# Performance work log

Measured on AMD Instinct MI355X. Metric: run time of the kernel, lower is better.

Reference implementation:

```python
import jax, jax.numpy as jnp
import numpy as np

N = 21  # nodes per graph (20 laser sectors + 1 robot node)
MAX_RANGE = 10.0
_bound = np.linspace(-np.pi / 2 - 0.03, np.pi / 2, 21, dtype=np.float32)[:-1]
_angles = _bound + np.float32(np.pi / 20)
ANGLE_FEAT = jnp.asarray(np.stack([np.sin(_angles), np.cos(_angles)], 1), dtype=jnp.float32)  # [20,2]


def _build_nodes(state24):
    # state24: [B,24] -> node features [B,21,7]
    B = state24.shape[0]
    laser = state24[:, :20, None] / MAX_RANGE                       # [B,20,1]
    angle = jnp.broadcast_to(ANGLE_FEAT[None], (B, 20, 2))          # [B,20,2]
    sector = jnp.concatenate([laser, angle, jnp.zeros((B, 20, 4), state24.dtype)], -1)  # [B,20,7]
    robot = jnp.concatenate([jnp.zeros((B, 1, 3), state24.dtype), state24[:, None, 20:]], -1)  # [B,1,7]
    return jnp.concatenate([sector, robot], axis=1)                 # [B,21,7]


def _gatv2(x, Wl, Wr, att, bias, heads, dim):
    # GATv2 over a fully-connected graph with self-loops (dense all-pairs).
    # e_ij = att . leaky_relu(Wl x_j + Wr x_i); alpha = softmax_j; out_i = sum_j alpha_ij (Wl x_j)
    B = x.shape[0]
    gl = (x @ Wl).reshape(B, N, heads, dim)  # source transform [B,j,H,D]
    gr = (x @ Wr).reshape(B, N, heads, dim)  # target transform [B,i,H,D]
    s = jax.nn.leaky_relu(gl[:, None] + gr[:, :, None], negative_slope=0.2)  # [B,i,j,H,D]
    e = jnp.einsum('bijhd,hd->bijh', s, att)                                  # [B,i,j,H]
    alpha = jax.nn.softmax(e, axis=2)                                          # softmax over sources j
    out = jnp.einsum('bijh,bjhd->bihd', alpha, gl).reshape(B, N, heads * dim)
    return out + bias


def setup_inputs() -> dict:
    key = jax.random.key(0)
    ks = jax.random.split(key, 16)
    r = lambda k, shape, s: (jax.random.normal(k, shape, dtype=jnp.float32) * s)
    B = 1024
    return {
        'state24': jax.random.normal(ks[0], (B, 24), dtype=jnp.float32),
        'Wl1': r(ks[1], (7, 256), 0.3), 'Wr1': r(ks[2], (7, 256), 0.3),
        'att1': r(ks[3], (4, 64), 0.1), 'b1': r(ks[4], (256,), 0.02),
        'Wl2': r(ks[5], (256, 64), 0.06), 'Wr2': r(ks[6], (256, 64), 0.06),
        'att2': r(ks[7], (1, 64), 0.1), 'b2': r(ks[8], (64,), 0.02),
        'fc1_w': r(ks[9], (64, 256), 0.12), 'fc1_b': r(ks[10], (256,), 0.02),
        'fc2_w': r(ks[11], (256, 256), 0.06), 'fc2_b': r(ks[12], (256,), 0.02),
        'fc3_w': r(ks[13], (256, 2), 0.06), 'fc3_b': r(ks[14], (2,), 0.02),
    }


def reference(state24, Wl1, Wr1, att1, b1, Wl2, Wr2, att2, b2,
              fc1_w, fc1_b, fc2_w, fc2_b, fc3_w, fc3_b):
    x = _build_nodes(state24)                               # [B,21,7]
    h = jax.nn.elu(_gatv2(x, Wl1, Wr1, att1, b1, 4, 64))    # [B,21,256]
    h = _gatv2(h, Wl2, Wr2, att2, b2, 1, 64)                # [B,21,64]
    nfv = jnp.mean(h, axis=1)                               # global_mean_pool -> [B,64]
    h = jax.nn.relu(nfv @ fc1_w + fc1_b)
    h = jax.nn.relu(h @ fc2_w + fc2_b)
    return jnp.tanh(h @ fc3_w + fc3_b)                      # [B,2]
```

## Files before the change

kernel.cpp:

```cpp
#include <hip/hip_runtime.h>
#include <hip/hip_fp16.h>
#include <math.h>

#define PI_D 3.141592653589793

typedef _Float16 h2 __attribute__((ext_vector_type(2)));
typedef _Float16 h8 __attribute__((ext_vector_type(8)));
typedef unsigned short us8 __attribute__((ext_vector_type(8)));
typedef __fp16 f16v2 __attribute__((ext_vector_type(2)));
typedef __fp16 f16v8 __attribute__((ext_vector_type(8)));
typedef float f32x4 __attribute__((ext_vector_type(4)));

#define STR1 264
#define STR2 66
#define STR2H 72
#define EPS 24
#define EPS2 24

static __device__ __forceinline__ h2 pack_h2(float a, float b) {
    return __builtin_bit_cast(h2, __builtin_amdgcn_cvt_pkrtz(a, b));
}

static __device__ __forceinline__ float fdot2(h2 a, h2 b, float c) {
    return __builtin_amdgcn_fdot2(__builtin_bit_cast(f16v2, a),
                                  __builtin_bit_cast(f16v2, b), c, false);
}

static __device__ __forceinline__ h8 habs8(h8 x) {
    us8 u = __builtin_bit_cast(us8, x);
    us8 m = {0x7fff, 0x7fff, 0x7fff, 0x7fff, 0x7fff, 0x7fff, 0x7fff, 0x7fff};
    return __builtin_bit_cast(h8, (us8)(u & m));
}

static __device__ __forceinline__ f32x4 mfma16(h8 a, h8 b, f32x4 c) {
    return __builtin_amdgcn_mfma_f32_16x16x32_f16(
        __builtin_bit_cast(f16v8, a), __builtin_bit_cast(f16v8, b), c, 0, 0, 0);
}

__global__ __launch_bounds__(256) void pack_weights_kernel(
    const float* __restrict__ Wl2, const float* __restrict__ Wr2,
    const float* __restrict__ fc1_w, const float* __restrict__ fc2_w,
    h8* __restrict__ ws)
{
    int idx = blockIdx.x * 256 + threadIdx.x;
    if (idx < 4096) {
        const float* W = idx < 2048 ? Wl2 : Wr2;
        int t = idx & 2047;
        int ntile = t >> 9, rem = t & 511;
        int kchunk = rem >> 6, lane = rem & 63;
        int n = ntile * 16 + (lane & 15);
        int k0 = kchunk * 32 + (lane >> 4) * 8;
        h8 o;
        #pragma unroll
        for (int j = 0; j < 8; ++j) o[j] = (_Float16)W[(k0 + j) * 64 + n];
        ws[idx] = o;
    } else if (idx < 6144) {
        int t = idx - 4096;
        int k2 = t >> 6, c = t & 63;
        h8 o;
        #pragma unroll
        for (int q = 0; q < 4; ++q) {
            o[2 * q]     = (_Float16)fc1_w[(2 * k2) * 256 + 4 * c + q];
            o[2 * q + 1] = (_Float16)fc1_w[(2 * k2 + 1) * 256 + 4 * c + q];
        }
        ws[idx] = o;
    } else {
        int t = idx - 6144;
        int k2 = t >> 6, c = t & 63;
        h8 o;
        #pragma unroll
        for (int q = 0; q < 4; ++q) {
            o[2 * q]     = (_Float16)fc2_w[(2 * k2) * 256 + 4 * c + q];
            o[2 * q + 1] = (_Float16)fc2_w[(2 * k2 + 1) * 256 + 4 * c + q];
        }
        ws[idx] = o;
    }
}

__global__ __launch_bounds__(256, 4) void actor_fused_kernel(
    const float* __restrict__ state24,
    const float* __restrict__ Wl1, const float* __restrict__ Wr1,
    const float* __restrict__ att1, const float* __restrict__ b1,
    const float* __restrict__ att2, const float* __restrict__ b2,
    const float* __restrict__ fc1_b, const float* __restrict__ fc2_b,
    const float* __restrict__ fc3_w, const float* __restrict__ fc3_b,
    const h8* __restrict__ wsL, const h8* __restrict__ wsR,
    const h8* __restrict__ wsF1, const h8* __restrict__ wsF2,
    float* __restrict__ out, int B)
{
    const int bix = blockIdx.x;
    if (bix >= B) return;
    const int tid = threadIdx.x;

    __shared__ float sinL[20], cosL[20], laserL[20], robotL[4];
    __shared__ __align__(16) h2 attLh[128];
    __shared__ __align__(16) h2 att2Lh[32];
    __shared__ __align__(16) _Float16 gr1h[22 * STR1];
    __shared__ __align__(16) union {
        struct { _Float16 gl1h[21 * STR1];
                 float eP[84 * EPS];
                 float uv[168]; } p1;
        struct { float gl2[24 * STR2];
                 _Float16 gl2h[24 * STR2H];
                 _Float16 gr2h[24 * STR2H];
                 float e2[24 * EPS2];
                 float u2v2[42];
                 float red[4][256];
                 _Float16 nfvh[64]; _Float16 hah[256]; _Float16 hbh[256]; } p2;
    } U;

    if (tid < 20) {
        double step = (PI_D + 0.03) / 20.0;
        float bound = (float)(-PI_D / 2.0 - 0.03 + (double)tid * step);
        float ang = bound + (float)(PI_D / 20.0);
        sinL[tid] = sinf(ang);
        cosL[tid] = cosf(ang);
        laserL[tid] = state24[bix * 24 + tid] * 0.1f;
    }
    if (tid >= 32 && tid < 36) robotL[tid - 32] = state24[bix * 24 + 20 + (tid - 32)];
    if (tid < 128) {
        float2 ap = ((const float2*)att1)[tid];
        attLh[tid] = pack_h2(0.4f * ap.x, 0.4f * ap.y);
    }
    if (tid >= 128 && tid < 160) {
        float2 ap = ((const float2*)att2)[tid - 128];
        att2Lh[tid - 128] = pack_h2(0.4f * ap.x, 0.4f * ap.y);
    }
    __syncthreads();

    {
        const int d2 = tid & 127;
        const int half = tid >> 7;
        float2 wl[7], wr[7];
        #pragma unroll
        for (int k = 0; k < 7; k++) {
            wl[k] = ((const float2*)Wl1)[k * 128 + d2];
            wr[k] = ((const float2*)Wr1)[k * 128 + d2];
        }
        const int base = half * 11;
        #pragma unroll
        for (int nn = 0; nn < 11; ++nn) {
            int node = base + nn;
            if (node < 21) {
                float a0, a1, b0, b1v;
                if (node < 20) {
                    float l = laserL[node], s = sinL[node], c = cosL[node];
                    a0 = l * wl[0].x + s * wl[1].x + c * wl[2].x;
                    a1 = l * wl[0].y + s * wl[1].y + c * wl[2].y;
                    b0 = l * wr[0].x + s * wr[1].x + c * wr[2].x;
                    b1v = l * wr[0].y + s * wr[1].y + c * wr[2].y;
                } else {
                    float r0 = robotL[0], r1 = robotL[1], r2 = robotL[2], r3 = robotL[3];
                    a0 = r0 * wl[3].x + r1 * wl[4].x + r2 * wl[5].x + r3 * wl[6].x;
                    a1 = r0 * wl[3].y + r1 * wl[4].y + r2 * wl[5].y + r3 * wl[6].y;
                    b0 = r0 * wr[3].x + r1 * wr[4].x + r2 * wr[5].x + r3 * wr[6].x;
                    b1v = r0 * wr[3].y + r1 * wr[4].y + r2 * wr[5].y + r3 * wr[6].y;
                }
                ((h2*)(U.p1.gl1h + node * STR1))[d2] = pack_h2(a0, a1);
                ((h2*)(gr1h + node * STR1))[d2] = pack_h2(b0, b1v);
            }
        }
    }
    __syncthreads();

    if (tid < 168) {
        int r = tid < 84 ? tid : tid - 84;
        int h = r / 21, idx = r - h * 21;
        const _Float16* rowp = (tid < 84 ? U.p1.gl1h : gr1h) + idx * STR1 + h * 64;
        const h8* row8 = (const h8*)rowp;
        const h2* ar = attLh + h * 32;
        float l0 = 0.f, l1 = 0.f;
        #pragma unroll
        for (int ch = 0; ch < 8; ++ch) {
            h8 g = row8[ch];
            l0 = fdot2(__builtin_shufflevector(g, g, 0, 1), ar[ch * 4 + 0], l0);
            l1 = fdot2(__builtin_shufflevector(g, g, 2, 3), ar[ch * 4 + 1], l1);
            l0 = fdot2(__builtin_shufflevector(g, g, 4, 5), ar[ch * 4 + 2], l0);
            l1 = fdot2(__builtin_shufflevector(g, g, 6, 7), ar[ch * 4 + 3], l1);
        }
        U.p1.uv[tid] = l0 + l1;
    }
    __syncthreads();

    {
        const int h = tid >> 6;
        const int lane = tid & 63;
        h2 ar[32];
        #pragma unroll
        for (int q = 0; q < 32; ++q) ar[q] = attLh[h * 32 + q];

        for (int it = 0; it < 7; ++it) {
            int q = it * 64 + lane;
            if (q < 441) {
                int i = q / 21;
                int j = q - i * 21;
                const h8* gA8 = (const h8*)(U.p1.gl1h + j * STR1 + h * 64);
                const h8* gB8 = (const h8*)(gr1h + i * STR1 + h * 64);
                float m0 = 0.f, m1 = 0.f;
                #pragma unroll
                for (int ch = 0; ch < 8; ++ch) {
                    h8 x = gA8[ch] + gB8[ch];
                    h8 ax = habs8(x);
                    m0 = fdot2(__builtin_shufflevector(ax, ax, 0, 1), ar[ch * 4 + 0], m0);
                    m1 = fdot2(__builtin_shufflevector(ax, ax, 2, 3), ar[ch * 4 + 1], m1);
                    m0 = fdot2(__builtin_shufflevector(ax, ax, 4, 5), ar[ch * 4 + 2], m0);
                    m1 = fdot2(__builtin_shufflevector(ax, ax, 6, 7), ar[ch * 4 + 3], m1);
                }
                U.p1.eP[(h * 21 + i) * EPS + j] = m0 + m1;
            }
        }
    }
    __syncthreads();

    if (tid < 84) {
        int h = tid / 21, i = tid - h * 21;
        float* row = U.p1.eP + tid * EPS;
        const float* uu = U.p1.uv + h * 21;
        float vi = 1.5f * U.p1.uv[84 + h * 21 + i];
        float ebuf[21];
        float m = -1e30f;
        #pragma unroll
        for (int j = 0; j < 21; j++) {
            float e = row[j] + 1.5f * uu[j] + vi;
            ebuf[j] = e;
            m = fmaxf(m, e);
        }
        float s = 0.f;
        #pragma unroll
        for (int j = 0; j < 21; j++) { float v = __expf(ebuf[j] - m); ebuf[j] = v; s += v; }
        float r = 1.f / s;
        #pragma unroll
        for (int j = 0; j < 21; j++) row[j] = ebuf[j] * r;
    }
    __syncthreads();

    {
        if (tid < 33) {
            h8 zz = {(_Float16)0.f, (_Float16)0.f, (_Float16)0.f, (_Float16)0.f,
                     (_Float16)0.f, (_Float16)0.f, (_Float16)0.f, (_Float16)0.f};
            ((h8*)gr1h)[21 * 33 + tid] = zz;
        }
        const int h = tid >> 6, c = tid & 63;
        const int col = h * 64 + c;
        float glv[21];
        #pragma unroll
        for (int j = 0; j < 21; ++j) glv[j] = (float)U.p1.gl1h[j * STR1 + col];
        float bb = b1[col];
        for (int i = 0; i < 21; ++i) {
            const float4* ar4 = (const float4*)(U.p1.eP + (h * 21 + i) * EPS);
            float4 q0 = ar4[0], q1 = ar4[1], q2 = ar4[2], q3 = ar4[3], q4 = ar4[4];
            float a20 = U.p1.eP[(h * 21 + i) * EPS + 20];
            float acc;
            acc = q0.x * glv[0];
            acc = fmaf(q0.y, glv[1], acc);
            acc = fmaf(q0.z, glv[2], acc);
            acc = fmaf(q0.w, glv[3], acc);
            acc = fmaf(q1.x, glv[4], acc);
            acc = fmaf(q1.y, glv[5], acc);
            acc = fmaf(q1.z, glv[6], acc);
            acc = fmaf(q1.w, glv[7], acc);
            acc = fmaf(q2.x, glv[8], acc);
            acc = fmaf(q2.y, glv[9], acc);
            acc = fmaf(q2.z, glv[10], acc);
            acc = fmaf(q2.w, glv[11], acc);
            acc = fmaf(q3.x, glv[12], acc);
            acc = fmaf(q3.y, glv[13], acc);
            acc = fmaf(q3.z, glv[14], acc);
            acc = fmaf(q3.w, glv[15], acc);
            acc = fmaf(q4.x, glv[16], acc);
            acc = fmaf(q4.y, glv[17], acc);
            acc = fmaf(q4.z, glv[18], acc);
            acc = fmaf(q4.w, glv[19], acc);
            acc = fmaf(a20, glv[20], acc);
            float v = acc + bb;
            v = v > 0.f ? v : __expf(v) - 1.f;
            gr1h[i * STR1 + col] = (_Float16)v;
        }
    }
    __syncthreads();

    {
        const int lane = tid & 63;
        const int w = tid >> 6;
        const int mrow = lane & 15;
        const int quad = lane >> 4;
        int rowA1 = 16 + mrow; if (rowA1 > 21) rowA1 = 21;
        const h8* hA0 = (const h8*)(gr1h + mrow * STR1 + quad * 8);
        const h8* hA1 = (const h8*)(gr1h + rowA1 * STR1 + quad * 8);
        const h8* bL = wsL + w * 512 + lane;
        const h8* bR = wsR + w * 512 + lane;
        f32x4 aL0 = {0.f, 0.f, 0.f, 0.f}, aL1 = {0.f, 0.f, 0.f, 0.f};
        f32x4 aR0 = {0.f, 0.f, 0.f, 0.f}, aR1 = {0.f, 0.f, 0.f, 0.f};
        #pragma unroll
        for (int kc = 0; kc < 8; ++kc) {
            h8 A0 = hA0[kc * 4];
            h8 A1 = hA1[kc * 4];
            h8 BL = bL[kc * 64];
            h8 BR = bR[kc * 64];
            aL0 = mfma16(A0, BL, aL0);
            aL1 = mfma16(A1, BL, aL1);
            aR0 = mfma16(A0, BR, aR0);
            aR1 = mfma16(A1, BR, aR1);
        }
        const int col = w * 16 + mrow;
        #pragma unroll
        for (int r = 0; r < 4; ++r) {
            int row0 = quad * 4 + r;
            U.p2.gl2[row0 * STR2 + col] = aL0[r];
            U.p2.gl2h[row0 * STR2H + col] = (_Float16)aL0[r];
            U.p2.gr2h[row0 * STR2H + col] = (_Float16)aR0[r];
            int row1 = 16 + row0;
            if (row1 < 21) {
                U.p2.gl2[row1 * STR2 + col] = aL1[r];
                U.p2.gl2h[row1 * STR2H + col] = (_Float16)aL1[r];
                U.p2.gr2h[row1 * STR2H + col] = (_Float16)aR1[r];
            }
        }
    }
    __syncthreads();

    {
        h2 ar2[32];
        #pragma unroll
        for (int q = 0; q < 32; ++q) ar2[q] = att2Lh[q];

        #pragma unroll
        for (int it = 0; it < 2; ++it) {
            int t = it * 256 + tid;
            if (t < 441) {
                int i = t / 21;
                int j = t - i * 21;
                const h8* gA8 = (const h8*)(U.p2.gl2h + j * STR2H);
                const h8* gB8 = (const h8*)(U.p2.gr2h + i * STR2H);
                float m0 = 0.f, m1 = 0.f;
                #pragma unroll
                for (int ch = 0; ch < 8; ++ch) {
                    h8 x = gA8[ch] + gB8[ch];
                    h8 ax = habs8(x);
                    m0 = fdot2(__builtin_shufflevector(ax, ax, 0, 1), ar2[ch * 4 + 0], m0);
                    m1 = fdot2(__builtin_shufflevector(ax, ax, 2, 3), ar2[ch * 4 + 1], m1);
                    m0 = fdot2(__builtin_shufflevector(ax, ax, 4, 5), ar2[ch * 4 + 2], m0);
                    m1 = fdot2(__builtin_shufflevector(ax, ax, 6, 7), ar2[ch * 4 + 3], m1);
                }
                U.p2.e2[i * EPS2 + j] = m0 + m1;
            } else if (t < 483) {
                int u = t - 441;
                int r = u < 21 ? u : u - 21;
                const _Float16* rowp = (u < 21 ? U.p2.gl2h : U.p2.gr2h) + r * STR2H;
                const h8* row8 = (const h8*)rowp;
                float l0 = 0.f, l1 = 0.f;
                #pragma unroll
                for (int ch = 0; ch < 8; ++ch) {
                    h8 g = row8[ch];
                    l0 = fdot2(__builtin_shufflevector(g, g, 0, 1), ar2[ch * 4 + 0], l0);
                    l1 = fdot2(__builtin_shufflevector(g, g, 2, 3), ar2[ch * 4 + 1], l1);
                    l0 = fdot2(__builtin_shufflevector(g, g, 4, 5), ar2[ch * 4 + 2], l0);
                    l1 = fdot2(__builtin_shufflevector(g, g, 6, 7), ar2[ch * 4 + 3], l1);
                }
                U.p2.u2v2[u] = l0 + l1;
            }
        }
    }
    __syncthreads();

    if (tid < 24) {
        float* row = U.p2.e2 + tid * EPS2;
        if (tid < 21) {
            const float* uu = U.p2.u2v2;
            float vi = 1.5f * U.p2.u2v2[21 + tid];
            float ebuf[21];
            float m = -1e30f;
            #pragma unroll
            for (int j = 0; j < 21; j++) {
                float e = row[j] + 1.5f * uu[j] + vi;
                ebuf[j] = e;
                m = fmaxf(m, e);
            }
            float s = 0.f;
            #pragma unroll
            for (int j = 0; j < 21; j++) { float v = __expf(ebuf[j] - m); ebuf[j] = v; s += v; }
            float r = 1.f / s;
            #pragma unroll
            for (int j = 0; j < 21; j++) row[j] = ebuf[j] * r;
        } else {
            #pragma unroll
            for (int j = 0; j < 21; j++) row[j] = 0.f;
        }
    }
    __syncthreads();

    {
        int d = tid & 63, g = tid >> 6;
        float glv2[21];
        #pragma unroll
        for (int j = 0; j < 21; ++j) glv2[j] = U.p2.gl2[j * STR2 + d];
        float sacc = 0.f;
        #pragma unroll
        for (int m = 0; m < 6; ++m) {
            int i = g + 4 * m;
            const float4* ar4 = (const float4*)(U.p2.e2 + i * EPS2);
            float4 q0 = ar4[0], q1 = ar4[1], q2 = ar4[2], q3 = ar4[3], q4 = ar4[4];
            float a20 = U.p2.e2[i * EPS2 + 20];
            float acc;
            acc = q0.x * glv2[0];
            acc = fmaf(q0.y, glv2[1], acc);
            acc = fmaf(q0.z, glv2[2], acc);
            acc = fmaf(q0.w, glv2[3], acc);
            acc = fmaf(q1.x, glv2[4], acc);
            acc = fmaf(q1.y, glv2[5], acc);
            acc = fmaf(q1.z, glv2[6], acc);
            acc = fmaf(q1.w, glv2[7], acc);
            acc = fmaf(q2.x, glv2[8], acc);
            acc = fmaf(q2.y, glv2[9], acc);
            acc = fmaf(q2.z, glv2[10], acc);
            acc = fmaf(q2.w, glv2[11], acc);
            acc = fmaf(q3.x, glv2[12], acc);
            acc = fmaf(q3.y, glv2[13], acc);
            acc = fmaf(q3.z, glv2[14], acc);
            acc = fmaf(q3.w, glv2[15], acc);
            acc = fmaf(q4.x, glv2[16], acc);
            acc = fmaf(q4.y, glv2[17], acc);
            acc = fmaf(q4.z, glv2[18], acc);
            acc = fmaf(q4.w, glv2[19], acc);
            acc = fmaf(a20, glv2[20], acc);
            sacc += acc;
        }
        U.p2.red[g][d] = sacc;
    }
    __syncthreads();
    if (tid < 64) {
        float v = (U.p2.red[0][tid] + U.p2.red[1][tid] + U.p2.red[2][tid] + U.p2.red[3][tid])
                  * (1.f / 21.f) + b2[tid];
        U.p2.nfvh[tid] = (_Float16)v;
    }
    __syncthreads();

    {
        int c = tid & 63, g = tid >> 6;
        const h2* x2p = (const h2*)U.p2.nfvh;
        float4 acc = {0.f, 0.f, 0.f, 0.f};
        #pragma unroll
        for (int kk = 0; kk < 8; ++kk) {
            int k2 = g * 8 + kk;
            h8 w = wsF1[k2 * 64 + c];
            h2 x2 = x2p[k2];
            acc.x = fdot2(__builtin_shufflevector(w, w, 0, 1), x2, acc.x);
            acc.y = fdot2(__builtin_shufflevector(w, w, 2, 3), x2, acc.y);
            acc.z = fdot2(__builtin_shufflevector(w, w, 4, 5), x2, acc.z);
            acc.w = fdot2(__builtin_shufflevector(w, w, 6, 7), x2, acc.w);
        }
        ((float4*)U.p2.red[g])[c] = acc;
    }
    __syncthreads();
    {
        float v = U.p2.red[0][tid] + U.p2.red[1][tid] + U.p2.red[2][tid] + U.p2.red[3][tid]
                  + fc1_b[tid];
        U.p2.hah[tid] = (_Float16)fmaxf(v, 0.f);
    }
    __syncthreads();

    {
        int c = tid & 63, g = tid >> 6;
        const h8* haH = (const h8*)U.p2.hah;
        float4 acc = {0.f, 0.f, 0.f, 0.f};
#define FC2_STEP(q, p)                                                          \
        {                                                                       \
            int k2 = g * 32 + (q) * 4 + (p);                                    \
            h8 w = wsF2[k2 * 64 + c];                                           \
            h2 x2 = __builtin_shufflevector(xa, xa, 2 * (p), 2 * (p) + 1);      \
            acc.x = fdot2(__builtin_shufflevector(w, w, 0, 1), x2, acc.x);      \
            acc.y = fdot2(__builtin_shufflevector(w, w, 2, 3), x2, acc.y);      \
            acc.z = fdot2(__builtin_shufflevector(w, w, 4, 5), x2, acc.z);      \
            acc.w = fdot2(__builtin_shufflevector(w, w, 6, 7), x2, acc.w);      \
        }
        #pragma unroll
        for (int q = 0; q < 8; ++q) {
            h8 xa = haH[g * 8 + q];
            FC2_STEP(q, 0)
            FC2_STEP(q, 1)
            FC2_STEP(q, 2)
            FC2_STEP(q, 3)
        }
#undef FC2_STEP
        ((float4*)U.p2.red[g])[c] = acc;
    }
    __syncthreads();
    {
        float v = U.p2.red[0][tid] + U.p2.red[1][tid] + U.p2.red[2][tid] + U.p2.red[3][tid]
                  + fc2_b[tid];
        U.p2.hbh[tid] = (_Float16)fmaxf(v, 0.f);
    }
    __syncthreads();

    if (tid < 128) {
        int o = tid >> 6, l = tid & 63;
        float s = 0.f;
        #pragma unroll
        for (int m = 0; m < 4; m++) {
            int k = l + 64 * m;
            s = fmaf((float)U.p2.hbh[k], fc3_w[k * 2 + o], s);
        }
        #pragma unroll
        for (int off = 32; off >= 1; off >>= 1) s += __shfl_down(s, off, 64);
        if (l == 0) out[bix * 2 + o] = tanhf(s + fc3_b[o]);
    }
}

extern "C" void kernel_launch(void* const* d_in, const int* in_sizes, int n_in,
                              void* d_out, int out_size, void* d_ws, size_t ws_size,
                              hipStream_t stream) {
    const float* state24 = (const float*)d_in[0];
    const float* Wl1 = (const float*)d_in[1];
    const float* Wr1 = (const float*)d_in[2];
    const float* att1 = (const float*)d_in[3];
    const float* b1 = (const float*)d_in[4];
    const float* Wl2 = (const float*)d_in[5];
    const float* Wr2 = (const float*)d_in[6];
    const float* att2 = (const float*)d_in[7];
    const float* b2 = (const float*)d_in[8];
    const float* fc1_w = (const float*)d_in[9];
    const float* fc1_b = (const float*)d_in[10];
    const float* fc2_w = (const float*)d_in[11];
    const float* fc2_b = (const float*)d_in[12];
    const float* fc3_w = (const float*)d_in[13];
    const float* fc3_b = (const float*)d_in[14];
    float* out = (float*)d_out;

    h8* ws = (h8*)d_ws;
    const h8* wsL = ws;
    const h8* wsR = ws + 2048;
    const h8* wsF1 = ws + 4096;
    const h8* wsF2 = ws + 6144;

    pack_weights_kernel<<<56, 256, 0, stream>>>(Wl2, Wr2, fc1_w, fc2_w, ws);

    int B = in_sizes[0] / 24;
    actor_fused_kernel<<<B, 256, 0, stream>>>(
        state24, Wl1, Wr1, att1, b1, att2, b2,
        fc1_b, fc2_b, fc3_w, fc3_b,
        wsL, wsR, wsF1, wsF2, out, B);
}
```

Measured before the change: 115.3 us.

## Use MFMA for GATv2 attention aggregation in both layers

Replaces the scalar FMA loops that compute alpha·gl in layers 1 and 2 with 16x16x32 f16 MFMA instructions. Softmax outputs are now written as zero-padded fp16 rows so they can serve directly as MFMA A operands, and layer 2 keeps a transposed fp16 copy of gl2 as the B operand. Layer 2 folds the mean pool into the MFMA output with shuffle reductions, which removes a barrier and a separate reduction stage. In exchange the attention weights and gl2 lose precision because they are held in fp16, and extra padding and zeroing stores are added.

New measurement: 115.8 us. About the same (+0.4%).

```diff
diff --git a/kernel.cpp b/kernel.cpp
--- a/kernel.cpp
+++ b/kernel.cpp
@@ -5,6 +5,7 @@
 #define PI_D 3.141592653589793
 
 typedef _Float16 h2 __attribute__((ext_vector_type(2)));
+typedef _Float16 h4 __attribute__((ext_vector_type(4)));
 typedef _Float16 h8 __attribute__((ext_vector_type(8)));
 typedef unsigned short us8 __attribute__((ext_vector_type(8)));
 typedef __fp16 f16v2 __attribute__((ext_vector_type(2)));
@@ -12,10 +13,7 @@
 typedef float f32x4 __attribute__((ext_vector_type(4)));
 
 #define STR1 264
-#define STR2 66
 #define STR2H 72
-#define EPS 24
-#define EPS2 24
 
 static __device__ __forceinline__ h2 pack_h2(float a, float b) {
     return __builtin_bit_cast(h2, __builtin_amdgcn_cvt_pkrtz(a, b));
@@ -97,13 +95,13 @@
     __shared__ __align__(16) h2 att2Lh[32];
     __shared__ __align__(16) _Float16 gr1h[22 * STR1];
     __shared__ __align__(16) union {
-        struct { _Float16 gl1h[21 * STR1];
-                 float eP[84 * EPS];
+        struct { _Float16 gl1h[22 * STR1];
+                 float ePf[128 * 24];
                  float uv[168]; } p1;
-        struct { float gl2[24 * STR2];
-                 _Float16 gl2h[24 * STR2H];
-                 _Float16 gr2h[24 * STR2H];
-                 float e2[24 * EPS2];
+        struct { _Float16 gl2h[21 * STR2H];
+                 _Float16 gr2h[21 * STR2H];
+                 _Float16 gl2hT[64 * 32];
+                 float e2[32 * 24];
                  float u2v2[42];
                  float red[4][256];
                  _Float16 nfvh[64]; _Float16 hah[256]; _Float16 hbh[256]; } p2;
@@ -129,6 +127,9 @@
     __syncthreads();
 
     {
+        h8 zz = {};
+        if (tid < 33) ((h8*)U.p1.gl1h)[21 * 33 + tid] = zz;
+
         const int d2 = tid & 127;
         const int half = tid >> 7;
         float2 wl[7], wr[7];
@@ -206,7 +207,7 @@
                     m0 = fdot2(__builtin_shufflevector(ax, ax, 4, 5), ar[ch * 4 + 2], m0);
                     m1 = fdot2(__builtin_shufflevector(ax, ax, 6, 7), ar[ch * 4 + 3], m1);
                 }
-                U.p1.eP[(h * 21 + i) * EPS + j] = m0 + m1;
+                U.p1.ePf[(h * 32 + i) * 24 + j] = m0 + m1;
             }
         }
     }
@@ -214,7 +215,8 @@
 
     if (tid < 84) {
         int h = tid / 21, i = tid - h * 21;
-        float* row = U.p1.eP + tid * EPS;
+        int r = h * 32 + i;
+        float* row = U.p1.ePf + r * 24;
         const float* uu = U.p1.uv + h * 21;
         float vi = 1.5f * U.p1.uv[84 + h * 21 + i];
         float ebuf[21];
@@ -228,53 +230,70 @@
         float s = 0.f;
         #pragma unroll
         for (int j = 0; j < 21; j++) { float v = __expf(ebuf[j] - m); ebuf[j] = v; s += v; }
-        float r = 1.f / s;
-        #pragma unroll
-        for (int j = 0; j < 21; j++) row[j] = ebuf[j] * r;
-    }
-    __syncthreads();
-
-    {
-        if (tid < 33) {
-            h8 zz = {(_Float16)0.f, (_Float16)0.f, (_Float16)0.f, (_Float16)0.f,
-                     (_Float16)0.f, (_Float16)0.f, (_Float16)0.f, (_Float16)0.f};
-            ((h8*)gr1h)[21 * 33 + tid] = zz;
-        }
-        const int h = tid >> 6, c = tid & 63;
-        const int col = h * 64 + c;
-        float glv[21];
-        #pragma unroll
-        for (int j = 0; j < 21; ++j) glv[j] = (float)U.p1.gl1h[j * STR1 + col];
-        float bb = b1[col];
-        for (int i = 0; i < 21; ++i) {
-            const float4* ar4 = (const float4*)(U.p1.eP + (h * 21 + i) * EPS);
-            float4 q0 = ar4[0], q1 = ar4[1], q2 = ar4[2], q3 = ar4[3], q4 = ar4[4];
-            float a20 = U.p1.eP[(h * 21 + i) * EPS + 20];
-            float acc;
-            acc = q0.x * glv[0];
-            acc = fmaf(q0.y, glv[1], acc);
-            acc = fmaf(q0.z, glv[2], acc);
-            acc = fmaf(q0.w, glv[3], acc);
-            acc = fmaf(q1.x, glv[4], acc);
-            acc = fmaf(q1.y, glv[5], acc);
-            acc = fmaf(q1.z, glv[6], acc);
-            acc = fmaf(q1.w, glv[7], acc);
-            acc = fmaf(q2.x, glv[8], acc);
-            acc = fmaf(q2.y, glv[9], acc);
-            acc = fmaf(q2.z, glv[10], acc);
-            acc = fmaf(q2.w, glv[11], acc);
-            acc = fmaf(q3.x, glv[12], acc);
-            acc = fmaf(q3.y, glv[13], acc);
-            acc = fmaf(q3.z, glv[14], acc);
-            acc = fmaf(q3.w, glv[15], acc);
-            acc = fmaf(q4.x, glv[16], acc);
-            acc = fmaf(q4.y, glv[17], acc);
-            acc = fmaf(q4.z, glv[18], acc);
-            acc = fmaf(q4.w, glv[19], acc);
-            acc = fmaf(a20, glv[20], acc);
-            float v = acc + bb;
-            v = v > 0.f ? v : __expf(v) - 1.f;
-            gr1h[i * STR1 + col] = (_Float16)v;
+        float rinv = 1.f / s;
+        h8* hp8 = (h8*)(U.p1.ePf) + r * 6;
+        h8 o0, o1, o2;
+        #pragma unroll
+        for (int q = 0; q < 8; ++q) o0[q] = (_Float16)(ebuf[q] * rinv);
+        #pragma unroll
+        for (int q = 0; q < 8; ++q) o1[q] = (_Float16)(ebuf[8 + q] * rinv);
+        #pragma unroll
+        for (int q = 0; q < 5; ++q) o2[q] = (_Float16)(ebuf[16 + q] * rinv);
+        o2[5] = (_Float16)0.f; o2[6] = (_Float16)0.f; o2[7] = (_Float16)0.f;
+        h8 zz = {};
+        hp8[0] = o0; hp8[1] = o1; hp8[2] = o2;
+        hp8[3] = zz; hp8[4] = zz; hp8[5] = zz;
+    } else {
+        h8 zz = {};
+        for (int z = tid - 84; z < 264; z += 172) {
+            int rr = z / 6, slot = z - rr * 6;
+            int h = rr / 11, m = 21 + (rr - h * 11);
+            ((h8*)U.p1.ePf)[(h * 32 + m) * 6 + slot] = zz;
+        }
+    }
+    __syncthreads();
+
+    {
+        h8 zz = {};
+        if (tid < 33) ((h8*)gr1h)[21 * 33 + tid] = zz;
+
+        const int lane = tid & 63;
+        const int h = tid >> 6;
+        const int mcol = lane & 15;
+        const int quad = lane >> 4;
+        const h8* Af = (const h8*)U.p1.ePf;
+        h8 A0 = Af[(h * 32 + mcol) * 6 + quad];
+        h8 A1 = Af[(h * 32 + 16 + mcol) * 6 + quad];
+        int rowoff[8];
+        #pragma unroll
+        for (int jj = 0; jj < 8; ++jj) {
+            int rr = quad * 8 + jj;
+            rowoff[jj] = (rr > 21 ? 21 : rr) * STR1;
+        }
+        const int colbase = h * 64 + mcol;
+        f32x4 z4 = {0.f, 0.f, 0.f, 0.f};
+        #pragma unroll
+        for (int t = 0; t < 4; ++t) {
+            int col = colbase + t * 16;
+            h8 bv;
+            #pragma unroll
+            for (int jj = 0; jj < 8; ++jj) bv[jj] = U.p1.gl1h[rowoff[jj] + col];
+            f32x4 d0 = mfma16(A0, bv, z4);
+            f32x4 d1 = mfma16(A1, bv, z4);
+            float bb = b1[col];
+            #pragma unroll
+            for (int r = 0; r < 4; ++r) {
+                int n0 = quad * 4 + r;
+                float v = d0[r] + bb;
+                v = v > 0.f ? v : __expf(v) - 1.f;
+                gr1h[n0 * STR1 + col] = (_Float16)v;
+                int n1 = 16 + quad * 4 + r;
+                if (n1 < 21) {
+                    float w2 = d1[r] + bb;
+                    w2 = w2 > 0.f ? w2 : __expf(w2) - 1.f;
+                    gr1h[n1 * STR1 + col] = (_Float16)w2;
+                }
+            }
         }
     }
     __syncthreads();
@@ -306,15 +325,27 @@
         #pragma unroll
         for (int r = 0; r < 4; ++r) {
             int row0 = quad * 4 + r;
-            U.p2.gl2[row0 * STR2 + col] = aL0[r];
             U.p2.gl2h[row0 * STR2H + col] = (_Float16)aL0[r];
             U.p2.gr2h[row0 * STR2H + col] = (_Float16)aR0[r];
             int row1 = 16 + row0;
             if (row1 < 21) {
-                U.p2.gl2[row1 * STR2 + col] = aL1[r];
                 U.p2.gl2h[row1 * STR2H + col] = (_Float16)aL1[r];
                 U.p2.gr2h[row1 * STR2H + col] = (_Float16)aR1[r];
             }
+        }
+        {
+            h2 lo0 = pack_h2(aL0[0], aL0[1]);
+            h2 hi0 = pack_h2(aL0[2], aL0[3]);
+            h4 p0 = __builtin_shufflevector(lo0, hi0, 0, 1, 2, 3);
+            *(h4*)(U.p2.gl2hT + col * 32 + quad * 4) = p0;
+            float m0v = (16 + quad * 4 + 0 < 21) ? aL1[0] : 0.f;
+            float m1v = (16 + quad * 4 + 1 < 21) ? aL1[1] : 0.f;
+            float m2v = (16 + quad * 4 + 2 < 21) ? aL1[2] : 0.f;
+            float m3v = (16 + quad * 4 + 3 < 21) ? aL1[3] : 0.f;
+            h2 lo1 = pack_h2(m0v, m1v);
+            h2 hi1 = pack_h2(m2v, m3v);
+            h4 p1 = __builtin_shufflevector(lo1, hi1, 0, 1, 2, 3);
+            *(h4*)(U.p2.gl2hT + col * 32 + 16 + quad * 4) = p1;
         }
     }
     __syncthreads();
@@ -342,7 +373,7 @@
                     m0 = fdot2(__builtin_shufflevector(ax, ax, 4, 5), ar2[ch * 4 + 2], m0);
                     m1 = fdot2(__builtin_shufflevector(ax, ax, 6, 7), ar2[ch * 4 + 3], m1);
                 }
-                U.p2.e2[i * EPS2 + j] = m0 + m1;
+                U.p2.e2[i * 24 + j] = m0 + m1;
             } else if (t < 483) {
                 int u = t - 441;
                 int r = u < 21 ? u : u - 21;
@@ -363,75 +394,62 @@
     }
     __syncthreads();
 
-    if (tid < 24) {
-        float* row = U.p2.e2 + tid * EPS2;
-        if (tid < 21) {
-            const float* uu = U.p2.u2v2;
-            float vi = 1.5f * U.p2.u2v2[21 + tid];
-            float ebuf[21];
-            float m = -1e30f;
-            #pragma unroll
-            for (int j = 0; j < 21; j++) {
-                float e = row[j] + 1.5f * uu[j] + vi;
-                ebuf[j] = e;
-                m = fmaxf(m, e);
-            }
-            float s = 0.f;
-            #pragma unroll
-            for (int j = 0; j < 21; j++) { float v = __expf(ebuf[j] - m); ebuf[j] = v; s += v; }
-            float r = 1.f / s;
-            #pragma unroll
-            for (int j = 0; j < 21; j++) row[j] = ebuf[j] * r;
-        } else {
-            #pragma unroll
-            for (int j = 0; j < 21; j++) row[j] = 0.f;
-        }
-    }
-    __syncthreads();
-
-    {
-        int d = tid & 63, g = tid >> 6;
-        float glv2[21];
-        #pragma unroll
-        for (int j = 0; j < 21; ++j) glv2[j] = U.p2.gl2[j * STR2 + d];
-        float sacc = 0.f;
-        #pragma unroll
-        for (int m = 0; m < 6; ++m) {
-            int i = g + 4 * m;
-            const float4* ar4 = (const float4*)(U.p2.e2 + i * EPS2);
-            float4 q0 = ar4[0], q1 = ar4[1], q2 = ar4[2], q3 = ar4[3], q4 = ar4[4];
-            float a20 = U.p2.e2[i * EPS2 + 20];
-            float acc;
-            acc = q0.x * glv2[0];
-            acc = fmaf(q0.y, glv2[1], acc);
-            acc = fmaf(q0.z, glv2[2], acc);
-            acc = fmaf(q0.w, glv2[3], acc);
-            acc = fmaf(q1.x, glv2[4], acc);
-            acc = fmaf(q1.y, glv2[5], acc);
-            acc = fmaf(q1.z, glv2[6], acc);
-            acc = fmaf(q1.w, glv2[7], acc);
-            acc = fmaf(q2.x, glv2[8], acc);
-            acc = fmaf(q2.y, glv2[9], acc);
-            acc = fmaf(q2.z, glv2[10], acc);
-            acc = fmaf(q2.w, glv2[11], acc);
-            acc = fmaf(q3.x, glv2[12], acc);
-            acc = fmaf(q3.y, glv2[13], acc);
-            acc = fmaf(q3.z, glv2[14], acc);
-            acc = fmaf(q3.w, glv2[15], acc);
-            acc = fmaf(q4.x, glv2[16], acc);
-            acc = fmaf(q4.y, glv2[17], acc);
-            acc = fmaf(q4.z, glv2[18], acc);
-            acc = fmaf(q4.w, glv2[19], acc);
-            acc = fmaf(a20, glv2[20], acc);
-            sacc += acc;
-        }
-        U.p2.red[g][d] = sacc;
-    }
-    __syncthreads();
-    if (tid < 64) {
-        float v = (U.p2.red[0][tid] + U.p2.red[1][tid] + U.p2.red[2][tid] + U.p2.red[3][tid])
-                  * (1.f / 21.f) + b2[tid];
-        U.p2.nfvh[tid] = (_Float16)v;
+    if (tid < 21) {
+        float* row = U.p2.e2 + tid * 24;
+        const float* uu = U.p2.u2v2;
+        float vi = 1.5f * U.p2.u2v2[21 + tid];
+        float ebuf[21];
+        float m = -1e30f;
+        #pragma unroll
+        for (int j = 0; j < 21; j++) {
+            float e = row[j] + 1.5f * uu[j] + vi;
+            ebuf[j] = e;
+            m = fmaxf(m, e);
+        }
+        float s = 0.f;
+        #pragma unroll
+        for (int j = 0; j < 21; j++) { float v = __expf(ebuf[j] - m); ebuf[j] = v; s += v; }
+        float rinv = 1.f / s;
+        h8* hp8 = (h8*)(U.p2.e2) + tid * 6;
+        h8 o0, o1, o2;
+        #pragma unroll
+        for (int q = 0; q < 8; ++q) o0[q] = (_Float16)(ebuf[q] * rinv);
+        #pragma unroll
+        for (int q = 0; q < 8; ++q) o1[q] = (_Float16)(ebuf[8 + q] * rinv);
+        #pragma unroll
+        for (int q = 0; q < 5; ++q) o2[q] = (_Float16)(ebuf[16 + q] * rinv);
+        o2[5] = (_Float16)0.f; o2[6] = (_Float16)0.f; o2[7] = (_Float16)0.f;
+        h8 zz = {};
+        hp8[0] = o0; hp8[1] = o1; hp8[2] = o2;
+        hp8[3] = zz; hp8[4] = zz; hp8[5] = zz;
+    } else if (tid < 87) {
+        int z = tid - 21;
+        int rr = z / 6, slot = z - rr * 6;
+        h8 zz = {};
+        ((h8*)U.p2.e2)[(21 + rr) * 6 + slot] = zz;
+    }
+    __syncthreads();
+
+    {
+        const int lane = tid & 63;
+        const int w = tid >> 6;
+        const int mcol = lane & 15;
+        const int quad = lane >> 4;
+        const h8* Af2 = (const h8*)U.p2.e2;
+        h8 A0 = Af2[mcol * 6 + quad];
+        h8 A1 = Af2[(16 + mcol) * 6 + quad];
+        h8 bv = *(const h8*)(U.p2.gl2hT + (w * 16 + mcol) * 32 + quad * 8);
+        f32x4 z4 = {0.f, 0.f, 0.f, 0.f};
+        f32x4 d0 = mfma16(A0, bv, z4);
+        f32x4 d1 = mfma16(A1, bv, z4);
+        float s = (d0[0] + d0[1]) + (d0[2] + d0[3])
+                + (d1[0] + d1[1]) + (d1[2] + d1[3]);
+        s += __shfl_xor(s, 16, 64);
+        s += __shfl_xor(s, 32, 64);
+        if (quad == 0) {
+            int col = w * 16 + mcol;
+            U.p2.nfvh[col] = (_Float16)(s * (1.f / 21.f) + b2[col]);
+        }
     }
     __syncthreads();
 
```
